# Kernel tuning notes

Hardware: AMD Instinct MI355X
Metric: run time of the kernel (lower is better)

Reference implementation:

```python
import jax, jax.numpy as jnp
import numpy as np

T, N, HIDDEN = 2048, 4, 512
N_HEAD = 8
D_HEAD = HIDDEN // N_HEAD
# Faithful to torch buffer: 1.0 / hidden_size ** d_head -> underflows to 0.0
SCALE = np.float32(1.0 / (HIDDEN ** D_HEAD))
LN_EPS = 1e-5


def _layernorm(x, g, b):
    m = jnp.mean(x, axis=-1, keepdims=True)
    v = jnp.mean(jnp.square(x - m), axis=-1, keepdims=True)
    return (x - m) * jax.lax.rsqrt(v + LN_EPS) * g + b


def setup_inputs() -> dict:
    key = jax.random.key(0)
    ks = jax.random.split(key, 6)
    s = 0.02
    return {
        "x": jax.random.normal(ks[0], (T, N, HIDDEN), jnp.float32),
        "qkv_w": jax.random.normal(ks[1], (HIDDEN, 3 * HIDDEN), jnp.float32) * s,
        "qkv_b": jnp.zeros((3 * HIDDEN,), jnp.float32),
        "out_w": jax.random.normal(ks[2], (HIDDEN, HIDDEN), jnp.float32) * s,
        "out_b": jnp.zeros((HIDDEN,), jnp.float32),
        "ln1_g": jnp.ones((HIDDEN,), jnp.float32),
        "ln1_b": jnp.zeros((HIDDEN,), jnp.float32),
        "ff1_w": jax.random.normal(ks[3], (HIDDEN, 2 * HIDDEN), jnp.float32) * s,
        "ff1_b": jnp.zeros((2 * HIDDEN,), jnp.float32),
        "ff2_w": jax.random.normal(ks[4], (2 * HIDDEN, HIDDEN), jnp.float32) * s,
        "ff2_b": jnp.zeros((HIDDEN,), jnp.float32),
        "ln2_g": jnp.ones((HIDDEN,), jnp.float32),
        "ln2_b": jnp.zeros((HIDDEN,), jnp.float32),
    }


def reference(x, qkv_w, qkv_b, out_w, out_b, ln1_g, ln1_b,
              ff1_w, ff1_b, ff2_w, ff2_b, ln2_g, ln2_b):
    t, n, _ = x.shape
    # prenorm=True path, dropout_p=0 (identity)
    residual = x
    h = _layernorm(x, ln1_g, ln1_b)
    qkv = h @ qkv_w + qkv_b  # [t, n, 3*hidden]
    q, k, v = jnp.split(qkv, 3, axis=2)
    q = q.reshape(t, n, N_HEAD, D_HEAD)
    k = k.reshape(t, n, N_HEAD, D_HEAD)
    v = v.reshape(t, n, N_HEAD, D_HEAD)
    logits = jnp.einsum('ibhd,jbhd->ijbh', q, k)
    probs = jax.nn.softmax(logits * SCALE, axis=1)
    attn_out = jnp.einsum('ijbh,jbhd->ibhd', probs, v).reshape(t, n, HIDDEN)
    x = residual + (attn_out @ out_w + out_b)
    residual = x
    h = _layernorm(x, ln2_g, ln2_b)
    ff = jnp.maximum(h @ ff1_w + ff1_b, 0.0) @ ff2_w + ff2_b
    return residual + ff
```

## Files before the change

### kernel.cpp

```cpp
#include <hip/hip_runtime.h>
#include <math.h>


#define DEVI __device__ __forceinline__

typedef unsigned short u16;
typedef unsigned int   u32;
using short8 = __attribute__((ext_vector_type(8))) short;
using f32x4  = __attribute__((ext_vector_type(4))) float;

constexpr int T_ = 2048;
constexpr int NB = 4;
constexpr int H  = 512;
constexpr int M  = T_ * NB;
constexpr int FF = 2 * H;
constexpr float LN_EPS = 1e-5f;
constexpr int NCHUNK = 256;

DEVI u16 f2bf(float f) {
    union { float f; u32 u; } v; v.f = f;
    u32 r = v.u + 0x7FFFu + ((v.u >> 16) & 1u);
    return (u16)(r >> 16);
}

DEVI void gload16(const u16* src, u16* lds) {
    __builtin_amdgcn_global_load_lds(
        (const __attribute__((address_space(1))) u32*)src,
        (__attribute__((address_space(3))) u32*)lds, 16, 0, 0);
}

DEVI float hsum8(const float4& a, const float4& b) {
    return a.x + a.y + a.z + a.w + b.x + b.y + b.z + b.w;
}
DEVI float hsq8(const float4& a, const float4& b) {
    return a.x*a.x + a.y*a.y + a.z*a.z + a.w*a.w +
           b.x*b.x + b.y*b.y + b.z*b.z + b.w*b.w;
}
DEVI float4 ln_apply(const float4& v, float mean, float rs,
                     const float4& g, const float4& b) {
    float4 r;
    r.x = (v.x - mean) * rs * g.x + b.x;
    r.y = (v.y - mean) * rs * g.y + b.y;
    r.z = (v.z - mean) * rs * g.z + b.z;
    r.w = (v.w - mean) * rs * g.w + b.w;
    return r;
}
DEVI void add4(float4& a, const float4& b) {
    a.x += b.x; a.y += b.y; a.z += b.z; a.w += b.w;
}
DEVI void wave_reduce2(float& s, float& q) {
    #pragma unroll
    for (int m = 1; m < 64; m <<= 1) {
        s += __shfl_xor(s, m, 64);
        q += __shfl_xor(q, m, 64);
    }
}

__global__ __launch_bounds__(256) void k_ln1_partial(
    const float* __restrict__ x, const float* __restrict__ g,
    const float* __restrict__ be, float* __restrict__ partials)
{
    const int lane = threadIdx.x & 63;
    const int w    = threadIdx.x >> 6;
    const int t0   = blockIdx.x * 8;

    const float4* G4 = (const float4*)g;
    const float4* B4 = (const float4*)be;
    const float4 g0 = G4[lane], g1 = G4[64 + lane];
    const float4 b0 = B4[lane], b1 = B4[64 + lane];

    float4 acc0 = {0, 0, 0, 0}, acc1 = {0, 0, 0, 0};
    for (int i = 0; i < 8; ++i) {
        const int r = (t0 + i) * NB + w;
        const float4* X4 = (const float4*)(x + (size_t)r * H);
        float4 v0 = X4[lane], v1 = X4[64 + lane];
        float s = hsum8(v0, v1);
        float q = hsq8(v0, v1);
        wave_reduce2(s, q);
        const float mean = s * (1.0f / H);
        const float var  = q * (1.0f / H) - mean * mean;
        const float rs   = 1.0f / sqrtf(var + LN_EPS);
        add4(acc0, ln_apply(v0, mean, rs, g0, b0));
        add4(acc1, ln_apply(v1, mean, rs, g1, b1));
    }
    float4* P4 = (float4*)(partials + ((size_t)w * NCHUNK + blockIdx.x) * H);
    P4[lane]      = acc0;
    P4[64 + lane] = acc1;
}

__global__ __launch_bounds__(256) void k_reduce_mean(
    const float* __restrict__ partials, float* __restrict__ mean_h1)
{
    const int tid = blockIdx.x * 256 + threadIdx.x;
    const int out = tid >> 3;
    const int sub = tid & 7;
    const int b = out >> 9;
    const int e = out & 511;
    float s = 0.f;
    #pragma unroll 8
    for (int i = 0; i < 32; ++i) {
        const int c = sub * 32 + i;
        s += partials[((size_t)b * NCHUNK + c) * H + e];
    }
    s += __shfl_xor(s, 1, 64);
    s += __shfl_xor(s, 2, 64);
    s += __shfl_xor(s, 4, 64);
    if (sub == 0) mean_h1[out] = s * (1.0f / T_);
}

__global__ __launch_bounds__(256) void k_gemv_tpo(
    const float* __restrict__ vec, const float* __restrict__ W,
    const float* __restrict__ bias, float* __restrict__ outv,
    const int Kd, const int rowstride, const int colofs)
{
    __shared__ float v[512];
    const int t = threadIdx.x;
    const int b = blockIdx.x >> 1;
    const int j = (blockIdx.x & 1) * 256 + t;
    for (int i = t; i < Kd; i += 256) v[i] = vec[(size_t)b * Kd + i];
    __syncthreads();
    float acc = bias[j];
    const float* wp = W + colofs + j;
    #pragma unroll 8
    for (int k = 0; k < Kd; ++k)
        acc = fmaf(v[k], wp[(size_t)k * rowstride], acc);
    outv[(size_t)b * 512 + j] = acc;
}

__global__ __launch_bounds__(256) void k_ln2(
    const float* __restrict__ x, const float* __restrict__ cvec,
    const float* __restrict__ g, const float* __restrict__ be,
    u16* __restrict__ h2f)
{
    const int lane = threadIdx.x & 63;
    const int w    = threadIdx.x >> 6;
    const int r    = blockIdx.x * 4 + w;
    const int b    = r & 3;

    const float4* X4 = (const float4*)(x + (size_t)r * H);
    const float4* C4 = (const float4*)(cvec + (size_t)b * H);
    float4 v0 = X4[lane * 2],     v1 = X4[lane * 2 + 1];
    add4(v0, C4[lane * 2]);
    add4(v1, C4[lane * 2 + 1]);

    float s = hsum8(v0, v1);
    float q = hsq8(v0, v1);
    wave_reduce2(s, q);
    const float mean = s * (1.0f / H);
    const float var  = q * (1.0f / H) - mean * mean;
    const float rs   = 1.0f / sqrtf(var + LN_EPS);

    const float4* G4 = (const float4*)g;
    const float4* B4 = (const float4*)be;
    float4 h0 = ln_apply(v0, mean, rs, G4[lane * 2],     B4[lane * 2]);
    float4 h1 = ln_apply(v1, mean, rs, G4[lane * 2 + 1], B4[lane * 2 + 1]);

    short8 o;
    o[0] = f2bf(h0.x); o[1] = f2bf(h0.y); o[2] = f2bf(h0.z); o[3] = f2bf(h0.w);
    o[4] = f2bf(h1.x); o[5] = f2bf(h1.y); o[6] = f2bf(h1.z); o[7] = f2bf(h1.w);

    const size_t idx = (((size_t)(r >> 4) * 16 + (lane >> 2)) << 9)
                     + ((lane & 3) * 16 + (r & 15)) * 8;
    *(short8*)&h2f[idx] = o;
}

__global__ __launch_bounds__(256) void k_wsplit(
    const float* __restrict__ W, u16* __restrict__ Wf,
    const int K, const int N)
{
    __shared__ float tile[32][33];
    const int k0 = blockIdx.x * 32, n0 = blockIdx.y * 32;
    const int t = threadIdx.x;
    const int KT = K >> 5;
    #pragma unroll
    for (int i = 0; i < 4; ++i) {
        const int idx = t + i * 256;
        const int r = idx >> 5, c = idx & 31;
        tile[r][c] = W[(size_t)(k0 + r) * N + n0 + c];
    }
    __syncthreads();
    if (t < 128) {
        const int tt = t >> 6;
        const int c  = t & 63;
        short8 o;
        #pragma unroll
        for (int kin = 0; kin < 8; ++kin)
            o[kin] = f2bf(tile[(c >> 4) * 8 + kin][tt * 16 + (c & 15)]);
        const size_t idx = (((size_t)(n0 / 16 + tt) * KT + (k0 >> 5)) << 9)
                         + c * 8;
        *(short8*)&Wf[idx] = o;
    }
}

template<int MODE>
__global__ __launch_bounds__(256) void gemm_bf16(
    const u16* __restrict__ Af, const u16* __restrict__ Bf,
    const float* __restrict__ bias,
    const float* __restrict__ resid_x, const float* __restrict__ resid_c,
    float* __restrict__ outf, u16* __restrict__ outfrag,
    const int K, const int N)
{
    constexpr int BM = 128, BN = 128, BK = 64;
    const int KT = K >> 5;
    __shared__ alignas(16) u16 As[BM * BK];
    __shared__ alignas(16) u16 Bs[BN * BK];

    const int t    = threadIdx.x;
    const int lane = t & 63, w = t >> 6;
    const int wr = w >> 1, wc = w & 1;
    const int lr = lane & 15, lk = lane >> 4;
    const int bmt = blockIdx.x * 8;
    const int bnt = blockIdx.y * 8;

    f32x4 acc[4][4];
    #pragma unroll
    for (int i = 0; i < 4; ++i)
        #pragma unroll
        for (int j = 0; j < 4; ++j)
            acc[i][j] = (f32x4){0.f, 0.f, 0.f, 0.f};

    for (int kt0 = 0; kt0 < KT; kt0 += 2) {
        __syncthreads();
        #pragma unroll
        for (int ft = 0; ft < 4; ++ft) {
            const int f = ft * 256 + t;
            const int mt = f >> 7, ktl = (f >> 6) & 1, c = f & 63;
            gload16(Af + (((size_t)(bmt + mt) * KT + kt0 + ktl) << 9) + c * 8,
                    &As[f * 8]);
        }
        #pragma unroll
        for (int ft = 0; ft < 4; ++ft) {
            const int f = ft * 256 + t;
            const int nt = f >> 7, ktl = (f >> 6) & 1, c = f & 63;
            gload16(Bf + (((size_t)(bnt + nt) * KT + kt0 + ktl) << 9) + c * 8,
                    &Bs[f * 8]);
        }
        __syncthreads();

        #pragma unroll
        for (int ktl = 0; ktl < 2; ++ktl) {
            short8 a[4], b[4];
            #pragma unroll
            for (int i = 0; i < 4; ++i)
                a[i] = *(const short8*)&As[(((wr * 4 + i) * 2 + ktl) << 9) + lane * 8];
            #pragma unroll
            for (int j = 0; j < 4; ++j)
                b[j] = *(const short8*)&Bs[(((wc * 4 + j) * 2 + ktl) << 9) + lane * 8];
            #pragma unroll
            for (int i = 0; i < 4; ++i)
                #pragma unroll
                for (int j = 0; j < 4; ++j)
                    acc[i][j] = __builtin_amdgcn_mfma_f32_16x16x32_bf16(
                        a[i], b[j], acc[i][j], 0, 0, 0);
        }
    }

    const int K2T = N >> 5;
    #pragma unroll
    for (int i = 0; i < 4; ++i) {
        const int rt   = bmt + wr * 4 + i;
        const int row0 = rt * 16 + lk * 4;
        #pragma unroll
        for (int j = 0; j < 4; ++j) {
            const int col = (bnt + wc * 4 + j) * 16 + lr;
            const float bv = bias[col];
            #pragma unroll
            for (int r = 0; r < 4; ++r) {
                const int row = row0 + r;
                float v = acc[i][j][r] + bv;
                if (MODE == 0) {
                    v = fmaxf(v, 0.f);
                    const size_t idx =
                        (((size_t)rt * K2T + (col >> 5)) << 9)
                        + (((col >> 3) & 3) * 16 + (lk * 4 + r)) * 8
                        + (col & 7);
                    outfrag[idx] = f2bf(v);
                } else {
                    v += resid_x[(size_t)row * N + col]
                       + resid_c[(row & 3) * N + col];
                    outf[(size_t)row * N + col] = v;
                }
            }
        }
    }
}

extern "C" void kernel_launch(void* const* d_in, const int* in_sizes, int n_in,
                              void* d_out, int out_size, void* d_ws, size_t ws_size,
                              hipStream_t stream)
{
    const float* x     = (const float*)d_in[0];
    const float* qkv_w = (const float*)d_in[1];
    const float* qkv_b = (const float*)d_in[2];
    const float* out_w = (const float*)d_in[3];
    const float* out_b = (const float*)d_in[4];
    const float* ln1_g = (const float*)d_in[5];
    const float* ln1_b = (const float*)d_in[6];
    const float* ff1_w = (const float*)d_in[7];
    const float* ff1_b = (const float*)d_in[8];
    const float* ff2_w = (const float*)d_in[9];
    const float* ff2_b = (const float*)d_in[10];
    const float* ln2_g = (const float*)d_in[11];
    const float* ln2_b = (const float*)d_in[12];

    float* out = (float*)d_out;

    float* fws      = (float*)d_ws;
    float* partials = fws;
    float* mh       = fws + (size_t)4 * NCHUNK * H;
    float* vmean    = mh + NB * H;
    float* cvec     = vmean + NB * H;
    u16*   h2f      = (u16*)(cvec + NB * H);
    u16*   f1f      = h2f + (size_t)M * H;
    u16*   w1f      = f1f + (size_t)M * FF;
    u16*   w2f      = w1f + (size_t)H * FF;

    k_wsplit<<<dim3(H / 32, FF / 32), 256, 0, stream>>>(ff1_w, w1f, H, FF);
    k_wsplit<<<dim3(FF / 32, H / 32), 256, 0, stream>>>(ff2_w, w2f, FF, H);

    k_ln1_partial<<<NCHUNK, 256, 0, stream>>>(x, ln1_g, ln1_b, partials);
    k_reduce_mean<<<64, 256, 0, stream>>>(partials, mh);
    k_gemv_tpo<<<8, 256, 0, stream>>>(mh, qkv_w, qkv_b + 2 * H, vmean,
                                      H, 3 * H, 2 * H);
    k_gemv_tpo<<<8, 256, 0, stream>>>(vmean, out_w, out_b, cvec,
                                      H, H, 0);

    k_ln2<<<M / 4, 256, 0, stream>>>(x, cvec, ln2_g, ln2_b, h2f);

    gemm_bf16<0><<<dim3(M / 128, FF / 128), 256, 0, stream>>>(
        h2f, w1f, ff1_b, nullptr, nullptr, nullptr, f1f, H, FF);

    gemm_bf16<1><<<dim3(M / 128, H / 128), 256, 0, stream>>>(
        f1f, w2f, ff2_b, x, cvec, out, nullptr, FF, H);
}
```

Measured before the change: 199.0 us.

## Merge weight prep kernels, atomically reduce LN1 mean, parallelize mean-path GEMVs

Merges the two weight bf16 split kernels into one launch, which also zeroes the mean buffer. LN1 partial sums are now reduced with global float atomics, removing the separate partials buffer and reduction kernel. The two GEMVs on the averaged vector now split K across threads in 128 blocks with an LDS reduction, replacing 8 blocks of serial loops. The aim is fewer launches and better parallelism on the small serial front-end, at the cost of atomic contention and a nondeterministic summation order.

```diff
diff --git a/kernel.cpp b/kernel.cpp
--- a/kernel.cpp
+++ b/kernel.cpp
@@ -15,7 +15,6 @@
 constexpr int M  = T_ * NB;
 constexpr int FF = 2 * H;
 constexpr float LN_EPS = 1e-5f;
-constexpr int NCHUNK = 256;
 
 DEVI u16 f2bf(float f) {
     union { float f; u32 u; } v; v.f = f;
@@ -56,9 +55,53 @@
     }
 }
 
-__global__ __launch_bounds__(256) void k_ln1_partial(
+__global__ __launch_bounds__(256) void k_prep(
+    const float* __restrict__ W1, const float* __restrict__ W2,
+    u16* __restrict__ w1f, u16* __restrict__ w2f, float* __restrict__ mh)
+{
+    __shared__ float tile[32][33];
+    const int t = threadIdx.x;
+    const int bid = blockIdx.x;
+
+    if (bid == 0) {
+        for (int i = t; i < NB * H; i += 256) mh[i] = 0.f;
+    }
+
+    const float* W;
+    u16* Wf;
+    int K, N, k0, n0;
+    if (bid < 512) {
+        W = W1; Wf = w1f; K = H; N = FF;
+        k0 = (bid & 15) * 32;  n0 = (bid >> 4) * 32;
+    } else {
+        const int b2 = bid - 512;
+        W = W2; Wf = w2f; K = FF; N = H;
+        k0 = (b2 & 31) * 32;   n0 = (b2 >> 5) * 32;
+    }
+
+    #pragma unroll
+    for (int i = 0; i < 4; ++i) {
+        const int idx = t + i * 256;
+        const int r = idx >> 5, c = idx & 31;
+        tile[r][c] = W[(size_t)(k0 + r) * N + n0 + c];
+    }
+    __syncthreads();
+    if (t < 128) {
+        const int tt = t >> 6;
+        const int c  = t & 63;
+        short8 o;
+        #pragma unroll
+        for (int kin = 0; kin < 8; ++kin)
+            o[kin] = f2bf(tile[(c >> 4) * 8 + kin][tt * 16 + (c & 15)]);
+        const size_t idx = (((size_t)(n0 / 16 + tt) * (K >> 5) + (k0 >> 5)) << 9)
+                         + c * 8;
+        *(short8*)&Wf[idx] = o;
+    }
+}
+
+__global__ __launch_bounds__(256) void k_ln1_atomic(
     const float* __restrict__ x, const float* __restrict__ g,
-    const float* __restrict__ be, float* __restrict__ partials)
+    const float* __restrict__ be, float* __restrict__ mh)
 {
     const int lane = threadIdx.x & 63;
     const int w    = threadIdx.x >> 6;
@@ -83,48 +126,43 @@
         add4(acc0, ln_apply(v0, mean, rs, g0, b0));
         add4(acc1, ln_apply(v1, mean, rs, g1, b1));
     }
-    float4* P4 = (float4*)(partials + ((size_t)w * NCHUNK + blockIdx.x) * H);
-    P4[lane]      = acc0;
-    P4[64 + lane] = acc1;
-}
-
-__global__ __launch_bounds__(256) void k_reduce_mean(
-    const float* __restrict__ partials, float* __restrict__ mean_h1)
-{
-    const int tid = blockIdx.x * 256 + threadIdx.x;
-    const int out = tid >> 3;
-    const int sub = tid & 7;
-    const int b = out >> 9;
-    const int e = out & 511;
-    float s = 0.f;
-    #pragma unroll 8
-    for (int i = 0; i < 32; ++i) {
-        const int c = sub * 32 + i;
-        s += partials[((size_t)b * NCHUNK + c) * H + e];
-    }
-    s += __shfl_xor(s, 1, 64);
-    s += __shfl_xor(s, 2, 64);
-    s += __shfl_xor(s, 4, 64);
-    if (sub == 0) mean_h1[out] = s * (1.0f / T_);
-}
-
-__global__ __launch_bounds__(256) void k_gemv_tpo(
+    float* dst = mh + (size_t)w * H;
+    atomicAdd(&dst[lane * 4 + 0],       acc0.x);
+    atomicAdd(&dst[lane * 4 + 1],       acc0.y);
+    atomicAdd(&dst[lane * 4 + 2],       acc0.z);
+    atomicAdd(&dst[lane * 4 + 3],       acc0.w);
+    atomicAdd(&dst[256 + lane * 4 + 0], acc1.x);
+    atomicAdd(&dst[256 + lane * 4 + 1], acc1.y);
+    atomicAdd(&dst[256 + lane * 4 + 2], acc1.z);
+    atomicAdd(&dst[256 + lane * 4 + 3], acc1.w);
+}
+
+__global__ __launch_bounds__(256) void k_gemv_coal(
     const float* __restrict__ vec, const float* __restrict__ W,
     const float* __restrict__ bias, float* __restrict__ outv,
-    const int Kd, const int rowstride, const int colofs)
-{
-    __shared__ float v[512];
-    const int t = threadIdx.x;
-    const int b = blockIdx.x >> 1;
-    const int j = (blockIdx.x & 1) * 256 + t;
-    for (int i = t; i < Kd; i += 256) v[i] = vec[(size_t)b * Kd + i];
+    const int Kd, const int stride, const int colofs, const float vscale)
+{
+    __shared__ float red[16][17];
+    const int t  = threadIdx.x;
+    const int b  = blockIdx.x >> 5;
+    const int j0 = (blockIdx.x & 31) * 16;
+    const int jj = t & 15, ks = t >> 4;
+
+    const float* vp = vec + (size_t)b * Kd + ks * 32;
+    const float* wp = W + (size_t)(ks * 32) * stride + colofs + j0 + jj;
+    float acc = 0.f;
+    #pragma unroll 8
+    for (int i = 0; i < 32; ++i)
+        acc = fmaf(vp[i] * vscale, wp[(size_t)i * stride], acc);
+
+    red[ks][jj] = acc;
     __syncthreads();
-    float acc = bias[j];
-    const float* wp = W + colofs + j;
-    #pragma unroll 8
-    for (int k = 0; k < Kd; ++k)
-        acc = fmaf(v[k], wp[(size_t)k * rowstride], acc);
-    outv[(size_t)b * 512 + j] = acc;
+    if (t < 16) {
+        float s = 0.f;
+        #pragma unroll
+        for (int k2 = 0; k2 < 16; ++k2) s += red[k2][t];
+        outv[(size_t)b * 512 + j0 + t] = s + bias[j0 + t];
+    }
 }
 
 __global__ __launch_bounds__(256) void k_ln2(
@@ -162,34 +200,6 @@
     const size_t idx = (((size_t)(r >> 4) * 16 + (lane >> 2)) << 9)
                      + ((lane & 3) * 16 + (r & 15)) * 8;
     *(short8*)&h2f[idx] = o;
-}
-
-__global__ __launch_bounds__(256) void k_wsplit(
-    const float* __restrict__ W, u16* __restrict__ Wf,
-    const int K, const int N)
-{
-    __shared__ float tile[32][33];
-    const int k0 = blockIdx.x * 32, n0 = blockIdx.y * 32;
-    const int t = threadIdx.x;
-    const int KT = K >> 5;
-    #pragma unroll
-    for (int i = 0; i < 4; ++i) {
-        const int idx = t + i * 256;
-        const int r = idx >> 5, c = idx & 31;
-        tile[r][c] = W[(size_t)(k0 + r) * N + n0 + c];
-    }
-    __syncthreads();
-    if (t < 128) {
-        const int tt = t >> 6;
-        const int c  = t & 63;
-        short8 o;
-        #pragma unroll
-        for (int kin = 0; kin < 8; ++kin)
-            o[kin] = f2bf(tile[(c >> 4) * 8 + kin][tt * 16 + (c & 15)]);
-        const size_t idx = (((size_t)(n0 / 16 + tt) * KT + (k0 >> 5)) << 9)
-                         + c * 8;
-        *(short8*)&Wf[idx] = o;
-    }
 }
 
 template<int MODE>
@@ -305,25 +315,23 @@
 
     float* out = (float*)d_out;
 
-    float* fws      = (float*)d_ws;
-    float* partials = fws;
-    float* mh       = fws + (size_t)4 * NCHUNK * H;
-    float* vmean    = mh + NB * H;
-    float* cvec     = vmean + NB * H;
-    u16*   h2f      = (u16*)(cvec + NB * H);
-    u16*   f1f      = h2f + (size_t)M * H;
-    u16*   w1f      = f1f + (size_t)M * FF;
-    u16*   w2f      = w1f + (size_t)H * FF;
-
-    k_wsplit<<<dim3(H / 32, FF / 32), 256, 0, stream>>>(ff1_w, w1f, H, FF);
-    k_wsplit<<<dim3(FF / 32, H / 32), 256, 0, stream>>>(ff2_w, w2f, FF, H);
-
-    k_ln1_partial<<<NCHUNK, 256, 0, stream>>>(x, ln1_g, ln1_b, partials);
-    k_reduce_mean<<<64, 256, 0, stream>>>(partials, mh);
-    k_gemv_tpo<<<8, 256, 0, stream>>>(mh, qkv_w, qkv_b + 2 * H, vmean,
-                                      H, 3 * H, 2 * H);
-    k_gemv_tpo<<<8, 256, 0, stream>>>(vmean, out_w, out_b, cvec,
-                                      H, H, 0);
+    float* fws   = (float*)d_ws;
+    float* mh    = fws;
+    float* vmean = mh + NB * H;
+    float* cvec  = vmean + NB * H;
+    u16*   h2f   = (u16*)(cvec + NB * H);
+    u16*   f1f   = h2f + (size_t)M * H;
+    u16*   w1f   = f1f + (size_t)M * FF;
+    u16*   w2f   = w1f + (size_t)H * FF;
+
+    k_prep<<<1024, 256, 0, stream>>>(ff1_w, ff2_w, w1f, w2f, mh);
+
+    k_ln1_atomic<<<256, 256, 0, stream>>>(x, ln1_g, ln1_b, mh);
+
+    k_gemv_coal<<<128, 256, 0, stream>>>(mh, qkv_w, qkv_b + 2 * H, vmean,
+                                         H, 3 * H, 2 * H, 1.0f / T_);
+    k_gemv_coal<<<128, 256, 0, stream>>>(vmean, out_w, out_b, cvec,
+                                         H, H, 0, 1.0f);
 
     k_ln2<<<M / 4, 256, 0, stream>>>(x, cvec, ln2_g, ln2_b, h2f);
 
```

After: 176.9 us. -11.1%, faster.
